# Optimization experiments

Hardware: AMD Instinct MI355X
Metric: run time of the kernel (lower is better)

## Reference

```python
import jax, jax.numpy as jnp
import numpy as np

D, L, G, B, T = 512, 2, 64, 64, 512  # n_dim, n_layers, n_gaussian, batch, seq_len


def lstm_cell(x, h, c, Wih, Whh, bih, bhh):
    # PyTorch gate order: input, forget, cell(g), output
    g = x @ Wih.T + bih + h @ Whh.T + bhh  # [B, 4D]
    i, f, gg, o = jnp.split(g, 4, axis=-1)
    c = jax.nn.sigmoid(f) * c + jax.nn.sigmoid(i) * jnp.tanh(gg)
    h = jax.nn.sigmoid(o) * jnp.tanh(c)
    return h, c


def encode(x, Wih, Whh, bih, bhh):
    n = x.shape[0]
    xt = jnp.transpose(x, (1, 0, 2))  # [T, B, D]
    hs, cs = [], []
    for l in range(L):
        def step(carry, xv, l=l):
            h, c = carry
            h, c = lstm_cell(xv, h, c, Wih[l], Whh[l], bih[l], bhh[l])
            return (h, c), h
        z = jnp.zeros((n, D), x.dtype)
        (hT, cT), xt = jax.lax.scan(step, (z, z), xt)
        hs.append(hT); cs.append(cT)
    return jnp.stack(hs), jnp.stack(cs)  # [L, B, D] each


def decode(prev0, h0, c0, Wih, Whh, bih, bhh, length):
    def step(carry, _):
        prev, h, c = carry
        x = prev
        nh, nc = [], []
        for l in range(L):
            hl, cl = lstm_cell(x, h[l], c[l], Wih[l], Whh[l], bih[l], bhh[l])
            nh.append(hl); nc.append(cl); x = hl
        return (x, jnp.stack(nh), jnp.stack(nc)), x
    _, ys = jax.lax.scan(step, (prev0, h0, c0), None, length=length)
    return jnp.transpose(ys, (1, 0, 2))  # [B, T, D]


def vae(h, muW, mub, sigW, sigb, outW, outb, eps):
    mu = jnp.einsum('lbd,lgd->lbg', h, muW) + mub[:, None, :]
    sig = jnp.einsum('lbd,lgd->lbg', h, sigW) + sigb[:, None, :]
    z = mu + eps * sig  # reparameterization
    out = jnp.einsum('lbg,ldg->lbd', z, outW) + outb[:, None, :]
    return out, mu, sig


def setup_inputs() -> dict:
    key = jax.random.key(0)
    ks = jax.random.split(key, 26)
    kk = 1.0 / np.sqrt(D)
    u = lambda i, shp: jax.random.uniform(ks[i], shp, jnp.float32, -kk, kk)
    return {
        "x": jax.random.normal(ks[0], (B, T, D), jnp.float32),
        "initial": jnp.zeros((1, D), jnp.float32),
        "enc_Wih": u(1, (L, 4 * D, D)), "enc_Whh": u(2, (L, 4 * D, D)),
        "enc_bih": u(3, (L, 4 * D)), "enc_bhh": u(4, (L, 4 * D)),
        "dec_Wih": u(5, (L, 4 * D, D)), "dec_Whh": u(6, (L, 4 * D, D)),
        "dec_bih": u(7, (L, 4 * D)), "dec_bhh": u(8, (L, 4 * D)),
        "h_mu_W": u(9, (L, G, D)), "h_mu_b": u(10, (L, G)),
        "h_sig_W": u(11, (L, G, D)), "h_sig_b": u(12, (L, G)),
        "h_out_W": u(13, (L, D, G)), "h_out_b": u(14, (L, D)),
        "c_mu_W": u(15, (L, G, D)), "c_mu_b": u(16, (L, G)),
        "c_sig_W": u(17, (L, G, D)), "c_sig_b": u(18, (L, G)),
        "c_out_W": u(19, (L, D, G)), "c_out_b": u(20, (L, D)),
        "eps_h": jax.random.normal(ks[21], (L, B, G), jnp.float32),
        "eps_c": jax.random.normal(ks[22], (L, B, G), jnp.float32),
    }


def reference(x, initial, enc_Wih, enc_Whh, enc_bih, enc_bhh,
              dec_Wih, dec_Whh, dec_bih, dec_bhh,
              h_mu_W, h_mu_b, h_sig_W, h_sig_b, h_out_W, h_out_b,
              c_mu_W, c_mu_b, c_sig_W, c_sig_b, c_out_W, c_out_b,
              eps_h, eps_c):
    h, c = encode(x, enc_Wih, enc_Whh, enc_bih, enc_bhh)
    h2, hmu, hsig = vae(h, h_mu_W, h_mu_b, h_sig_W, h_sig_b, h_out_W, h_out_b, eps_h)
    c2, cmu, csig = vae(c, c_mu_W, c_mu_b, c_sig_W, c_sig_b, c_out_W, c_out_b, eps_c)
    prev0 = jnp.broadcast_to(initial, (x.shape[0], D))
    out = decode(prev0, h2, c2, dec_Wih, dec_Whh, dec_bih, dec_bhh, x.shape[1])
    return out, jnp.concatenate([hmu, cmu], 0), jnp.concatenate([hsig, csig], 0)
```

## Files before the change

kernel.cpp:

```cpp
#include <hip/hip_runtime.h>
#include <hip/hip_bf16.h>

typedef __bf16 bf16_t;
typedef __attribute__((ext_vector_type(8))) __bf16 bf16x8;
typedef __attribute__((ext_vector_type(4))) float f32x4;
typedef __attribute__((ext_vector_type(4))) int i32x4;

#define MFMA16(a, b, c) __builtin_amdgcn_mfma_f32_16x16x32_bf16((a), (b), (c), 0, 0, 0)

namespace {
constexpr int TSEQ = 512, DDIM = 512, NB = 64;
constexpr size_t OFF_ENC_HBUF = 0;
constexpr size_t OFF_DEC_HBUF = 262144;
constexpr size_t OFF_DEC_YBUF = 524288;
constexpr size_t OFF_HT       = 655360;
constexpr size_t OFF_CT       = 917504;
constexpr size_t OFF_H2       = 1179648;
constexpr size_t OFF_C2       = 1441792;
constexpr int RETRY_CAP = 1 << 14;
template <int V> struct IC { static constexpr int v = V; };
}

__device__ __forceinline__ float sigm_f(float x) { return 1.f / (1.f + __expf(-x)); }
__device__ __forceinline__ float tanh_f(float x) {
  x = fminf(15.f, fmaxf(-15.f, x));
  const float e = __expf(-2.f * x);
  return (1.f - e) / (1.f + e);
}
__device__ __forceinline__ bf16x8 cvt8(const float* __restrict__ p) {
  const float4 a = *(const float4*)p;
  const float4 b = *(const float4*)(p + 4);
  bf16x8 r;
  r[0] = (bf16_t)a.x; r[1] = (bf16_t)a.y; r[2] = (bf16_t)a.z; r[3] = (bf16_t)a.w;
  r[4] = (bf16_t)b.x; r[5] = (bf16_t)b.y; r[6] = (bf16_t)b.z; r[7] = (bf16_t)b.w;
  return r;
}

union FRAG { i32x4 i; bf16x8 v; };

__device__ __forceinline__ unsigned tagpat(int g) {
  return ((((g + 1) >> 1) & 1) ^ 1) ? 0x00010001u : 0u;
}
__device__ __forceinline__ unsigned chk4(const i32x4& v, unsigned pat) {
  unsigned bad = 0;
#pragma unroll
  for (int j = 0; j < 4; ++j) bad |= ((unsigned)v[j] ^ pat) & 0x00010001u;
  return bad;
}

__device__ __forceinline__ void ldg_issue(const bf16_t* p, i32x4& d) {
  asm volatile("global_load_dwordx4 %0, %1, off sc0 sc1" : "=v"(d) : "v"(p) : "memory");
}
__device__ __forceinline__ void vm_wait0() {
  asm volatile("s_waitcnt vmcnt(0)" ::: "memory");
  __builtin_amdgcn_sched_barrier(0);
}
__device__ __forceinline__ void stg_tag(bf16_t* p, float a, float b, unsigned pat) {
  union { bf16_t h[2]; unsigned u; } x;
  x.h[0] = (bf16_t)a; x.h[1] = (bf16_t)b;
  __hip_atomic_store((unsigned*)p, (x.u & ~0x00010001u) | pat,
                     __ATOMIC_RELAXED, __HIP_MEMORY_SCOPE_AGENT);
}

__device__ __forceinline__ void load_weights(const float* Wih, const float* Whh,
                                             int wave, int c15, int kg, int d0,
                                             bf16x8 (&wA)[2][8], bf16x8 (&wB)[2][8]) {
  const float* Wsrc = (wave < 2) ? Wih : Whh;
  const int kb = (wave & 1) << 8;
#pragma unroll
  for (int l = 0; l < 2; ++l)
#pragma unroll
    for (int nt = 0; nt < 2; ++nt)
#pragma unroll
      for (int ks = 0; ks < 8; ++ks) {
        const int n = nt * 16 + c15;
        const int grow = (n >> 3) * DDIM + d0 + (n & 7);
        const float* p = Wsrc + (size_t)(l * 2048 + grow) * DDIM + kb + ks * 32 + kg * 8;
        if (nt == 0) wA[l][ks] = cvt8(p);
        else         wB[l][ks] = cvt8(p);
      }
}

__global__ __launch_bounds__(256, 1) void enc_pass(
    const float* __restrict__ x,
    const float* __restrict__ Wih, const float* __restrict__ Whh,
    const float* __restrict__ bih, const float* __restrict__ bhh,
    bf16_t* __restrict__ hbuf, float* __restrict__ hT, float* __restrict__ cT) {
  const int wg = blockIdx.x;
  const int grp = wg >> 6, slc = wg & 63;
  const int tid = threadIdx.x;
  const int wave = tid >> 6, lane = tid & 63;
  const int b0 = grp << 4, d0 = slc << 3;

  __shared__ float gbuf[2][4][16][33];
  __shared__ float bias_l[2][32];

  const int c15 = lane & 15, kg = lane >> 4;
  const int b = b0 + c15;

  bf16x8 wA[2][8], wB[2][8];
  load_weights(Wih, Whh, wave, c15, kg, d0, wA, wB);
  if (tid < 64) {
    const int l = tid >> 5, n = tid & 31;
    const int grow = (n >> 3) * DDIM + d0 + (n & 7);
    bias_l[l][n] = bih[l * 2048 + grow] + bhh[l * 2048 + grow];
  }
  if (tid < 128) {
    const int l = tid >> 6, r6 = tid & 63, rw = r6 >> 2, dp = r6 & 3;
    const int slot = (l == 0) ? 1 : 0;
    stg_tag(&hbuf[((size_t)(l * 2 + slot) * NB + b0 + rw) * DDIM + d0 + 2 * dp],
            0.f, 0.f, 0x00010001u);
  }
  __syncthreads();

  float cA = 0.f, cB = 0.f;

  for (int s = 0; s <= TSEQ; ++s) {
    const int p = s & 1, rp = p ^ 1;
    const unsigned patold = tagpat(s - 1);
    f32x4 pa0 = {0.f, 0.f, 0.f, 0.f}, pa1 = {0.f, 0.f, 0.f, 0.f};
    if (wave < 2 && s < TSEQ) {
      const int kq = wave << 8;
      const float* ap = x + ((size_t)b * TSEQ + s) * DDIM + kq + kg * 8;
#pragma unroll
      for (int ks = 0; ks < 8; ++ks) {
        const bf16x8 a = cvt8(ap + ks * 32);
        pa0 = MFMA16(a, wA[0][ks], pa0);
        pa1 = MFMA16(a, wB[0][ks], pa1);
      }
    }
    __syncthreads();
    if (wave >= 2) {
      const int kq = (wave - 2) << 8;
      FRAG f0[8], f1[8];
      const bf16_t* a0p = hbuf + ((size_t)(0 * 2 + rp) * NB + b) * DDIM + kq + kg * 8;
      const bf16_t* a1p = hbuf + ((size_t)(1 * 2 + rp) * NB + b) * DDIM + kq + kg * 8;
      int guard = 0;
      for (;;) {
        if (s < TSEQ) {
#pragma unroll
          for (int ks = 0; ks < 8; ++ks) ldg_issue(a0p + ks * 32, f0[ks].i);
        }
        if (s >= 1) {
#pragma unroll
          for (int ks = 0; ks < 8; ++ks) ldg_issue(a1p + ks * 32, f1[ks].i);
        }
        vm_wait0();
        unsigned bad = 0;
        if (s < TSEQ) {
#pragma unroll
          for (int ks = 0; ks < 8; ++ks) bad |= chk4(f0[ks].i, patold);
        }
        if (s >= 1) {
#pragma unroll
          for (int ks = 0; ks < 8; ++ks) bad |= chk4(f1[ks].i, patold);
        }
        if (__all(bad == 0) || ++guard > RETRY_CAP) break;
      }
      if (s < TSEQ) {
        f32x4 a0 = {0.f, 0.f, 0.f, 0.f}, a1 = {0.f, 0.f, 0.f, 0.f};
#pragma unroll
        for (int ks = 0; ks < 8; ++ks) {
          a0 = MFMA16(f0[ks].v, wA[0][ks], a0);
          a1 = MFMA16(f0[ks].v, wB[0][ks], a1);
        }
#pragma unroll
        for (int r = 0; r < 4; ++r) {
          gbuf[0][wave][kg * 4 + r][c15] = a0[r];
          gbuf[0][wave][kg * 4 + r][16 + c15] = a1[r];
        }
      }
      if (s >= 1) {
        f32x4 a0 = {0.f, 0.f, 0.f, 0.f}, a1 = {0.f, 0.f, 0.f, 0.f};
#pragma unroll
        for (int ks = 0; ks < 8; ++ks) {
          a0 = MFMA16(f1[ks].v, wA[1][ks], a0);
          a1 = MFMA16(f1[ks].v, wB[1][ks], a1);
        }
#pragma unroll
        for (int r = 0; r < 4; ++r) {
          gbuf[1][wave][kg * 4 + r][c15] = a0[r];
          gbuf[1][wave][kg * 4 + r][16 + c15] = a1[r];
        }
      }
    } else {
      if (s < TSEQ) {
#pragma unroll
        for (int r = 0; r < 4; ++r) {
          gbuf[0][wave][kg * 4 + r][c15] = pa0[r];
          gbuf[0][wave][kg * 4 + r][16 + c15] = pa1[r];
        }
      }
      if (s >= 1) {
        const int kq = wave << 8;
        FRAG f[8];
        const bf16_t* ap = hbuf + ((size_t)(0 * 2 + rp) * NB + b) * DDIM + kq + kg * 8;
        int guard = 0;
        for (;;) {
#pragma unroll
          for (int ks = 0; ks < 8; ++ks) ldg_issue(ap + ks * 32, f[ks].i);
          vm_wait0();
          unsigned bad = 0;
#pragma unroll
          for (int ks = 0; ks < 8; ++ks) bad |= chk4(f[ks].i, patold);
          if (__all(bad == 0) || ++guard > RETRY_CAP) break;
        }
        f32x4 a0 = {0.f, 0.f, 0.f, 0.f}, a1 = {0.f, 0.f, 0.f, 0.f};
#pragma unroll
        for (int ks = 0; ks < 8; ++ks) {
          a0 = MFMA16(f[ks].v, wA[1][ks], a0);
          a1 = MFMA16(f[ks].v, wB[1][ks], a1);
        }
#pragma unroll
        for (int r = 0; r < 4; ++r) {
          gbuf[1][wave][kg * 4 + r][c15] = a0[r];
          gbuf[1][wave][kg * 4 + r][16 + c15] = a1[r];
        }
      }
    }
    __syncthreads();
    if (tid < 128) {
      const int ll = tid >> 6, r6 = tid & 63, rw = r6 >> 2, dp = r6 & 3;
      const bool act = (ll == 0) ? (s < TSEQ) : (s >= 1);
      if (act) {
        const unsigned pat = tagpat(s);
        float hv2[2], cv2[2];
#pragma unroll
        for (int e2 = 0; e2 < 2; ++e2) {
          const int e = dp * 2 + e2;
          float gi = bias_l[ll][e],      gf = bias_l[ll][8 + e];
          float gg = bias_l[ll][16 + e], go = bias_l[ll][24 + e];
#pragma unroll
          for (int q = 0; q < 4; ++q) {
            gi += gbuf[ll][q][rw][e];
            gf += gbuf[ll][q][rw][8 + e];
            gg += gbuf[ll][q][rw][16 + e];
            go += gbuf[ll][q][rw][24 + e];
          }
          const float iv = sigm_f(gi), fv = sigm_f(gf), gv = tanh_f(gg), ov = sigm_f(go);
          float& cs = (e2 == 0) ? cA : cB;
          cs = fv * cs + iv * gv;
          cv2[e2] = cs;
          hv2[e2] = ov * tanh_f(cs);
        }
        const int b2 = b0 + rw, dc = d0 + dp * 2;
        stg_tag(&hbuf[((size_t)(ll * 2 + p) * NB + b2) * DDIM + dc], hv2[0], hv2[1], pat);
        if ((ll == 0 && s == TSEQ - 1) || (ll == 1 && s == TSEQ)) {
          *(float2*)&hT[((size_t)ll * NB + b2) * DDIM + dc] = float2{hv2[0], hv2[1]};
          *(float2*)&cT[((size_t)ll * NB + b2) * DDIM + dc] = float2{cv2[0], cv2[1]};
        }
      }
    }
  }
}

__global__ __launch_bounds__(256, 1) void dec_pass(
    const float* __restrict__ initial,
    const float* __restrict__ Wih, const float* __restrict__ Whh,
    const float* __restrict__ bih, const float* __restrict__ bhh,
    const float* __restrict__ h_init, const float* __restrict__ c_init,
    bf16_t* __restrict__ hbuf, bf16_t* __restrict__ ybuf,
    float* __restrict__ out) {
  const int wg = blockIdx.x;
  const int grp = wg >> 6, slc = wg & 63;
  const int tid = threadIdx.x;
  const int wave = tid >> 6, lane = tid & 63;
  const int b0 = grp << 4, d0 = slc << 3;

  __shared__ float gbuf[4][16][33];
  __shared__ float bias_l[2][32];

  const int c15 = lane & 15, kg = lane >> 4;
  const int b = b0 + c15;

  bf16x8 wA[2][8], wB[2][8];
  load_weights(Wih, Whh, wave, c15, kg, d0, wA, wB);
  if (tid < 64) {
    const int l = tid >> 5, n = tid & 31;
    const int grow = (n >> 3) * DDIM + d0 + (n & 7);
    bias_l[l][n] = bih[l * 2048 + grow] + bhh[l * 2048 + grow];
  }
  if (tid < 128) {
    const int l = tid >> 6, r6 = tid & 63, rw = r6 >> 2, dp = r6 & 3;
    const int b2 = b0 + rw, dc = d0 + 2 * dp;
    const float2 hv = *(const float2*)&h_init[((size_t)l * NB + b2) * DDIM + dc];
    stg_tag(&hbuf[((size_t)(l * 2 + 1) * NB + b2) * DDIM + dc], hv.x, hv.y, 0x00010001u);
  }
  if (tid < 64) {
    const int rw = tid >> 2, dp = tid & 3;
    const int dc = d0 + 2 * dp;
    stg_tag(&ybuf[((size_t)1 * NB + b0 + rw) * DDIM + dc], initial[dc], initial[dc + 1],
            0x00010001u);
  }
  const int rw0 = lane >> 2, dp0 = lane & 3;
  float cA0 = 0.f, cB0 = 0.f, cA1 = 0.f, cB1 = 0.f;
  if (wave == 0) {
    const float2 c0 = *(const float2*)&c_init[((size_t)0 * NB + b0 + rw0) * DDIM + d0 + 2 * dp0];
    const float2 c1 = *(const float2*)&c_init[((size_t)1 * NB + b0 + rw0) * DDIM + d0 + 2 * dp0];
    cA0 = c0.x; cB0 = c0.y; cA1 = c1.x; cB1 = c1.y;
  }
  __syncthreads();

  auto level = [&](auto lcc, const int t, const int p, const int rp) {
    constexpr int LC = decltype(lcc)::v;
    const unsigned patold = tagpat(t - 1);
    f32x4 pa0 = {0.f, 0.f, 0.f, 0.f}, pa1 = {0.f, 0.f, 0.f, 0.f};
    if (wave >= 2) {
      const int kq = (wave - 2) << 8;
      FRAG f[8];
      const bf16_t* ap = hbuf + ((size_t)(LC * 2 + rp) * NB + b) * DDIM + kq + kg * 8;
      int guard = 0;
      for (;;) {
#pragma unroll
        for (int ks = 0; ks < 8; ++ks) ldg_issue(ap + ks * 32, f[ks].i);
        vm_wait0();
        unsigned bad = 0;
#pragma unroll
        for (int ks = 0; ks < 8; ++ks) bad |= chk4(f[ks].i, patold);
        if (__all(bad == 0) || ++guard > RETRY_CAP) break;
      }
#pragma unroll
      for (int ks = 0; ks < 8; ++ks) {
        pa0 = MFMA16(f[ks].v, wA[LC][ks], pa0);
        pa1 = MFMA16(f[ks].v, wB[LC][ks], pa1);
      }
    }
    __syncthreads();
    if (wave >= 2) {
#pragma unroll
      for (int r = 0; r < 4; ++r) {
        gbuf[wave][kg * 4 + r][c15] = pa0[r];
        gbuf[wave][kg * 4 + r][16 + c15] = pa1[r];
      }
    } else {
      const int kq = wave << 8;
      const unsigned patf = (LC == 0) ? patold : tagpat(t);
      const bf16_t* base = (LC == 0) ? (ybuf + (size_t)rp * NB * DDIM)
                                     : (hbuf + (size_t)(0 * 2 + p) * NB * DDIM);
      const bf16_t* ap = base + (size_t)b * DDIM + kq + kg * 8;
      FRAG f[8];
      int guard = 0;
      for (;;) {
#pragma unroll
        for (int ks = 0; ks < 8; ++ks) ldg_issue(ap + ks * 32, f[ks].i);
        vm_wait0();
        unsigned bad = 0;
#pragma unroll
        for (int ks = 0; ks < 8; ++ks) bad |= chk4(f[ks].i, patf);
        if (__all(bad == 0) || ++guard > RETRY_CAP) break;
      }
      f32x4 a0 = {0.f, 0.f, 0.f, 0.f}, a1 = {0.f, 0.f, 0.f, 0.f};
#pragma unroll
      for (int ks = 0; ks < 8; ++ks) {
        a0 = MFMA16(f[ks].v, wA[LC][ks], a0);
        a1 = MFMA16(f[ks].v, wB[LC][ks], a1);
      }
#pragma unroll
      for (int r = 0; r < 4; ++r) {
        gbuf[wave][kg * 4 + r][c15] = a0[r];
        gbuf[wave][kg * 4 + r][16 + c15] = a1[r];
      }
    }
    __syncthreads();
    if (tid < 64) {
      const unsigned pat = tagpat(t);
      float hv2[2];
#pragma unroll
      for (int e2 = 0; e2 < 2; ++e2) {
        const int e = dp0 * 2 + e2;
        float gi = bias_l[LC][e],      gf = bias_l[LC][8 + e];
        float gg = bias_l[LC][16 + e], go = bias_l[LC][24 + e];
#pragma unroll
        for (int q = 0; q < 4; ++q) {
          gi += gbuf[q][rw0][e];
          gf += gbuf[q][rw0][8 + e];
          gg += gbuf[q][rw0][16 + e];
          go += gbuf[q][rw0][24 + e];
        }
        const float iv = sigm_f(gi), fv = sigm_f(gf), gv = tanh_f(gg), ov = sigm_f(go);
        float& cs = (LC == 0) ? ((e2 == 0) ? cA0 : cB0) : ((e2 == 0) ? cA1 : cB1);
        cs = fv * cs + iv * gv;
        hv2[e2] = ov * tanh_f(cs);
      }
      const int b2 = b0 + rw0, dc = d0 + dp0 * 2;
      stg_tag(&hbuf[((size_t)(LC * 2 + p) * NB + b2) * DDIM + dc], hv2[0], hv2[1], pat);
      if (LC == 1) {
        stg_tag(&ybuf[((size_t)p * NB + b2) * DDIM + dc], hv2[0], hv2[1], pat);
        *(float2*)&out[((size_t)b2 * TSEQ + t) * DDIM + dc] = float2{hv2[0], hv2[1]};
      }
    }
  };

  for (int t = 0; t < TSEQ; ++t) {
    const int p = t & 1, rp = p ^ 1;
    level(IC<0>{}, t, p, rp);
    level(IC<1>{}, t, p, rp);
  }
}

__global__ __launch_bounds__(512) void vae_kernel(
    const float* __restrict__ hT, const float* __restrict__ cT,
    const float* __restrict__ hmuW, const float* __restrict__ hmub,
    const float* __restrict__ hsigW, const float* __restrict__ hsigb,
    const float* __restrict__ houtW, const float* __restrict__ houtb,
    const float* __restrict__ cmuW, const float* __restrict__ cmub,
    const float* __restrict__ csigW, const float* __restrict__ csigb,
    const float* __restrict__ coutW, const float* __restrict__ coutb,
    const float* __restrict__ eps_h, const float* __restrict__ eps_c,
    float* __restrict__ h2, float* __restrict__ c2, float* __restrict__ out) {
  const int bid = blockIdx.x;
  const int b = bid & 63;
  const int l = (bid >> 6) & 1;
  const int hc = bid >> 7;
  const int tid = threadIdx.x;

  const float* S    = (hc ? cT : hT) + (l * 64 + b) * 512;
  const float* muW  = (hc ? cmuW : hmuW) + l * 64 * 512;
  const float* mub  = (hc ? cmub : hmub) + l * 64;
  const float* sigW = (hc ? csigW : hsigW) + l * 64 * 512;
  const float* sigb = (hc ? csigb : hsigb) + l * 64;
  const float* outW = (hc ? coutW : houtW) + l * 512 * 64;
  const float* outb = (hc ? coutb : houtb) + l * 512;
  const float* eps  = (hc ? eps_c : eps_h) + (l * 64 + b) * 64;
  float* S2 = (hc ? c2 : h2) + (l * 64 + b) * 512;

  __shared__ float srow[512];
  __shared__ float z[64];
  srow[tid] = S[tid];
  __syncthreads();
  if (tid < 64) {
    const float* wm = muW + tid * 512;
    const float* ws = sigW + tid * 512;
    float mu = mub[tid], sg = sigb[tid];
    for (int d = 0; d < 512; ++d) {
      mu = fmaf(srow[d], wm[d], mu);
      sg = fmaf(srow[d], ws[d], sg);
    }
    z[tid] = mu + eps[tid] * sg;
    const size_t base = (size_t)64 * 512 * 512;
    const size_t idx = ((size_t)(hc * 2 + l) * 64 + b) * 64 + tid;
    out[base + idx] = mu;
    out[base + 4 * 64 * 64 + idx] = sg;
  }
  __syncthreads();
  {
    const float* wo = outW + tid * 64;
    float acc = outb[tid];
#pragma unroll 8
    for (int g = 0; g < 64; ++g) acc = fmaf(z[g], wo[g], acc);
    S2[tid] = acc;
  }
}

extern "C" void kernel_launch(void* const* d_in, const int* in_sizes, int n_in,
                              void* d_out, int out_size, void* d_ws, size_t ws_size,
                              hipStream_t stream) {
  const float* x       = (const float*)d_in[0];
  const float* initial = (const float*)d_in[1];
  const float* eWih    = (const float*)d_in[2];
  const float* eWhh    = (const float*)d_in[3];
  const float* ebih    = (const float*)d_in[4];
  const float* ebhh    = (const float*)d_in[5];
  const float* dWih    = (const float*)d_in[6];
  const float* dWhh    = (const float*)d_in[7];
  const float* dbih    = (const float*)d_in[8];
  const float* dbhh    = (const float*)d_in[9];
  const float* hmuW    = (const float*)d_in[10];
  const float* hmub    = (const float*)d_in[11];
  const float* hsigW   = (const float*)d_in[12];
  const float* hsigb   = (const float*)d_in[13];
  const float* houtW   = (const float*)d_in[14];
  const float* houtb   = (const float*)d_in[15];
  const float* cmuW    = (const float*)d_in[16];
  const float* cmub    = (const float*)d_in[17];
  const float* csigW   = (const float*)d_in[18];
  const float* csigb   = (const float*)d_in[19];
  const float* coutW   = (const float*)d_in[20];
  const float* coutb   = (const float*)d_in[21];
  const float* eps_h   = (const float*)d_in[22];
  const float* eps_c   = (const float*)d_in[23];

  char* ws = (char*)d_ws;
  bf16_t* enc_hbuf = (bf16_t*)(ws + OFF_ENC_HBUF);
  bf16_t* dec_hbuf = (bf16_t*)(ws + OFF_DEC_HBUF);
  bf16_t* dec_ybuf = (bf16_t*)(ws + OFF_DEC_YBUF);
  float* hT = (float*)(ws + OFF_HT);
  float* cT = (float*)(ws + OFF_CT);
  float* h2 = (float*)(ws + OFF_H2);
  float* c2 = (float*)(ws + OFF_C2);
  float* out = (float*)d_out;

  hipMemsetAsync(ws, 0, OFF_HT, stream);

  enc_pass<<<256, 256, 0, stream>>>(x, eWih, eWhh, ebih, ebhh, enc_hbuf, hT, cT);
  vae_kernel<<<256, 512, 0, stream>>>(hT, cT, hmuW, hmub, hsigW, hsigb, houtW, houtb,
                                      cmuW, cmub, csigW, csigb, coutW, coutb,
                                      eps_h, eps_c, h2, c2, out);
  dec_pass<<<256, 256, 0, stream>>>(initial, dWih, dWhh, dbih, dbhh,
                                    h2, c2, dec_hbuf, dec_ybuf, out);
}
```

Measured before the change: 5.200 ms.

## Precompute encoder layer-0 input projection in a parallel pre-pass kernel

```diff
diff --git a/kernel.cpp b/kernel.cpp
--- a/kernel.cpp
+++ b/kernel.cpp
@@ -17,6 +17,8 @@
 constexpr size_t OFF_CT       = 917504;
 constexpr size_t OFF_H2       = 1179648;
 constexpr size_t OFF_C2       = 1441792;
+constexpr size_t OFF_GX       = 2097152;
+constexpr size_t GX_BYTES     = (size_t)512 * 256 * 256 * 4;
 constexpr int RETRY_CAP = 1 << 14;
 template <int V> struct IC { static constexpr int v = V; };
 }
@@ -81,11 +83,75 @@
       }
 }
 
+__global__ __launch_bounds__(256, 4) void gx_pass(
+    const float* __restrict__ x, const float* __restrict__ Wih,
+    unsigned* __restrict__ gx) {
+  const int wg0 = blockIdx.x & 255;
+  const int tc  = blockIdx.x >> 8;
+  const int grp = wg0 >> 6, slc = wg0 & 63;
+  const int tid = threadIdx.x;
+  const int wave = tid >> 6, lane = tid & 63;
+  const int c15 = lane & 15, kg = lane >> 4;
+  const int b0 = grp << 4, d0 = slc << 3;
+  const int kb = (wave & 1) << 8;
+  const int tpar = wave >> 1;
+
+  __shared__ float gbuf[2][2][16][33];
+
+  bf16x8 wA[8], wB[8];
+#pragma unroll
+  for (int nt = 0; nt < 2; ++nt)
+#pragma unroll
+    for (int ks = 0; ks < 8; ++ks) {
+      const int n = nt * 16 + c15;
+      const int grow = (n >> 3) * DDIM + d0 + (n & 7);
+      const float* p = Wih + (size_t)grow * DDIM + kb + ks * 32 + kg * 8;
+      if (nt == 0) wA[ks] = cvt8(p);
+      else         wB[ks] = cvt8(p);
+    }
+
+  const int b = b0 + c15;
+  for (int j = 0; j < 32; ++j) {
+    const int t = tc * 64 + 2 * j + tpar;
+    f32x4 a0 = {0.f, 0.f, 0.f, 0.f}, a1 = {0.f, 0.f, 0.f, 0.f};
+    const float* ap = x + ((size_t)b * TSEQ + t) * DDIM + kb + kg * 8;
+#pragma unroll
+    for (int ks = 0; ks < 8; ++ks) {
+      const bf16x8 a = cvt8(ap + ks * 32);
+      a0 = MFMA16(a, wA[ks], a0);
+      a1 = MFMA16(a, wB[ks], a1);
+    }
+#pragma unroll
+    for (int r = 0; r < 4; ++r) {
+      gbuf[tpar][wave & 1][kg * 4 + r][c15] = a0[r];
+      gbuf[tpar][wave & 1][kg * 4 + r][16 + c15] = a1[r];
+    }
+    __syncthreads();
+    if (tid < 128) {
+      const int ll = tid >> 6, r6 = tid & 63, rw = r6 >> 2, dp = r6 & 3;
+      const int tt = tc * 64 + 2 * j + ll;
+      const size_t base = ((size_t)tt * 256 + wg0) * 256 + rw * 16 + dp;
+#pragma unroll
+      for (int g = 0; g < 4; ++g) {
+        const int e = g * 8 + 2 * dp;
+        const float v0 = gbuf[ll][0][rw][e] + gbuf[ll][1][rw][e];
+        const float v1 = gbuf[ll][0][rw][e + 1] + gbuf[ll][1][rw][e + 1];
+        union { _Float16 h[2]; unsigned u; } pk;
+        pk.h[0] = (_Float16)v0; pk.h[1] = (_Float16)v1;
+        gx[base + g * 4] = pk.u;
+      }
+    }
+    __syncthreads();
+  }
+}
+
+template <int GX>
 __global__ __launch_bounds__(256, 1) void enc_pass(
     const float* __restrict__ x,
     const float* __restrict__ Wih, const float* __restrict__ Whh,
     const float* __restrict__ bih, const float* __restrict__ bhh,
-    bf16_t* __restrict__ hbuf, float* __restrict__ hT, float* __restrict__ cT) {
+    bf16_t* __restrict__ hbuf, float* __restrict__ hT, float* __restrict__ cT,
+    const unsigned* __restrict__ gx) {
   const int wg = blockIdx.x;
   const int grp = wg >> 6, slc = wg & 63;
   const int tid = threadIdx.x;
@@ -119,14 +185,23 @@
     const int p = s & 1, rp = p ^ 1;
     const unsigned patold = tagpat(s - 1);
     f32x4 pa0 = {0.f, 0.f, 0.f, 0.f}, pa1 = {0.f, 0.f, 0.f, 0.f};
-    if (wave < 2 && s < TSEQ) {
-      const int kq = wave << 8;
-      const float* ap = x + ((size_t)b * TSEQ + s) * DDIM + kq + kg * 8;
-#pragma unroll
-      for (int ks = 0; ks < 8; ++ks) {
-        const bf16x8 a = cvt8(ap + ks * 32);
-        pa0 = MFMA16(a, wA[0][ks], pa0);
-        pa1 = MFMA16(a, wB[0][ks], pa1);
+    unsigned gxr[4];
+    if constexpr (GX) {
+      if (tid < 64 && s < TSEQ) {
+        const size_t base = ((size_t)s * 256 + wg) * 256 + (tid >> 2) * 16 + (tid & 3);
+#pragma unroll
+        for (int g = 0; g < 4; ++g) gxr[g] = gx[base + g * 4];
+      }
+    } else {
+      if (wave < 2 && s < TSEQ) {
+        const int kq = wave << 8;
+        const float* ap = x + ((size_t)b * TSEQ + s) * DDIM + kq + kg * 8;
+#pragma unroll
+        for (int ks = 0; ks < 8; ++ks) {
+          const bf16x8 a = cvt8(ap + ks * 32);
+          pa0 = MFMA16(a, wA[0][ks], pa0);
+          pa1 = MFMA16(a, wB[0][ks], pa1);
+        }
       }
     }
     __syncthreads();
@@ -184,11 +259,13 @@
         }
       }
     } else {
-      if (s < TSEQ) {
-#pragma unroll
-        for (int r = 0; r < 4; ++r) {
-          gbuf[0][wave][kg * 4 + r][c15] = pa0[r];
-          gbuf[0][wave][kg * 4 + r][16 + c15] = pa1[r];
+      if constexpr (!GX) {
+        if (s < TSEQ) {
+#pragma unroll
+          for (int r = 0; r < 4; ++r) {
+            gbuf[0][wave][kg * 4 + r][c15] = pa0[r];
+            gbuf[0][wave][kg * 4 + r][16 + c15] = pa1[r];
+          }
         }
       }
       if (s >= 1) {
@@ -224,20 +301,38 @@
       const bool act = (ll == 0) ? (s < TSEQ) : (s >= 1);
       if (act) {
         const unsigned pat = tagpat(s);
+        float gs[4][2];
+#pragma unroll
+        for (int g = 0; g < 4; ++g) {
+          gs[g][0] = bias_l[ll][g * 8 + 2 * dp];
+          gs[g][1] = bias_l[ll][g * 8 + 2 * dp + 1];
+        }
+        if (GX && ll == 0) {
+#pragma unroll
+          for (int g = 0; g < 4; ++g) {
+            union { unsigned u; _Float16 h[2]; } dk;
+            dk.u = gxr[g];
+            gs[g][0] += (float)dk.h[0];
+            gs[g][1] += (float)dk.h[1];
+          }
+        }
+        const int q0 = (GX && ll == 0) ? 2 : 0;
+#pragma unroll
+        for (int q = 0; q < 4; ++q) {
+          if (q >= q0) {
+#pragma unroll
+            for (int g = 0; g < 4; ++g) {
+              const int e = g * 8 + 2 * dp;
+              gs[g][0] += gbuf[ll][q][rw][e];
+              gs[g][1] += gbuf[ll][q][rw][e + 1];
+            }
+          }
+        }
         float hv2[2], cv2[2];
 #pragma unroll
         for (int e2 = 0; e2 < 2; ++e2) {
-          const int e = dp * 2 + e2;
-          float gi = bias_l[ll][e],      gf = bias_l[ll][8 + e];
-          float gg = bias_l[ll][16 + e], go = bias_l[ll][24 + e];
-#pragma unroll
-          for (int q = 0; q < 4; ++q) {
-            gi += gbuf[ll][q][rw][e];
-            gf += gbuf[ll][q][rw][8 + e];
-            gg += gbuf[ll][q][rw][16 + e];
-            go += gbuf[ll][q][rw][24 + e];
-          }
-          const float iv = sigm_f(gi), fv = sigm_f(gf), gv = tanh_f(gg), ov = sigm_f(go);
+          const float iv = sigm_f(gs[0][e2]), fv = sigm_f(gs[1][e2]);
+          const float gv = tanh_f(gs[2][e2]), ov = sigm_f(gs[3][e2]);
           float& cs = (e2 == 0) ? cA : cB;
           cs = fv * cs + iv * gv;
           cv2[e2] = cs;
@@ -488,11 +583,18 @@
   float* cT = (float*)(ws + OFF_CT);
   float* h2 = (float*)(ws + OFF_H2);
   float* c2 = (float*)(ws + OFF_C2);
+  unsigned* gx = (unsigned*)(ws + OFF_GX);
   float* out = (float*)d_out;
 
   hipMemsetAsync(ws, 0, OFF_HT, stream);
 
-  enc_pass<<<256, 256, 0, stream>>>(x, eWih, eWhh, ebih, ebhh, enc_hbuf, hT, cT);
+  const bool use_gx = (ws_size >= OFF_GX + GX_BYTES);
+  if (use_gx) {
+    gx_pass<<<2048, 256, 0, stream>>>(x, eWih, gx);
+    enc_pass<1><<<256, 256, 0, stream>>>(x, eWih, eWhh, ebih, ebhh, enc_hbuf, hT, cT, gx);
+  } else {
+    enc_pass<0><<<256, 256, 0, stream>>>(x, eWih, eWhh, ebih, ebhh, enc_hbuf, hT, cT, nullptr);
+  }
   vae_kernel<<<256, 512, 0, stream>>>(hT, cT, hmuW, hmub, hsigW, hsigb, houtW, houtb,
                                       cmuW, cmub, csigW, csigb, coutW, coutb,
                                       eps_h, eps_c, h2, c2, out);
```

Result: faster. 4.918 ms (-5.4%).
